# Kernel optimization log

Measured on AMD Instinct MI355X. Metric: run time of the kernel, lower is better.

Reference implementation:

```python
import jax, jax.numpy as jnp
import numpy as np

B, N, E, D, H, OUT = 4, 20000, 320000, 64, 128, 64
EPS = 1e-5


def layernorm(x, g, b):
    m = x.mean(-1, keepdims=True)
    v = x.var(-1, keepdims=True)
    return (x - m) / jnp.sqrt(v + EPS) * g + b


def setup_inputs() -> dict:
    key = jax.random.key(0)
    ks = jax.random.split(key, 20)
    nodes = jax.random.normal(ks[0], (B, N, D), jnp.float32)
    edges = jax.random.randint(ks[1], (B, E, 2), 0, N)
    edge_weights = jax.random.uniform(ks[2], (B, E), dtype=jnp.float32)
    s = 0.05
    inp = {"nodes": nodes, "edges": edges, "edge_weights": edge_weights}
    dims = [(3 * D, H), (H, H), (H, H), (H, OUT)]
    for i, (di, do) in enumerate(dims, start=1):
        inp[f"W{i}"] = jax.random.normal(ks[2 + 4 * i], (di, do), jnp.float32) * s
        inp[f"b{i}"] = jax.random.normal(ks[3 + 4 * i], (do,), jnp.float32) * s
        inp[f"g{i}"] = 1.0 + jax.random.normal(ks[4 + 4 * i], (do,), jnp.float32) * s
        inp[f"t{i}"] = jax.random.normal(ks[5 + 4 * i], (do,), jnp.float32) * s
    return inp


def reference(nodes, edges, edge_weights,
              W1, b1, g1, t1, W2, b2, g2, t2,
              W3, b3, g3, t3, W4, b4, g4, t4):
    # gather source/dest node features per edge: [B, E, D]
    src_idx = edges[..., 0]  # [B, E]
    dst_idx = edges[..., 1]  # [B, E]
    w = edge_weights[..., None]  # [B, E, 1]
    in_feat = jnp.take_along_axis(nodes, src_idx[..., None], axis=1) * w
    out_feat = jnp.take_along_axis(nodes, dst_idx[..., None], axis=1) * w

    # scatter-sum per node (segment sum over flattened batch*node ids)
    off = jnp.arange(B, dtype=dst_idx.dtype)[:, None] * N
    agg_in = jax.ops.segment_sum(in_feat.reshape(B * E, D),
                                 (dst_idx + off).reshape(-1),
                                 num_segments=B * N).reshape(B, N, D)
    agg_out = jax.ops.segment_sum(out_feat.reshape(B * E, D),
                                  (src_idx + off).reshape(-1),
                                  num_segments=B * N).reshape(B, N, D)

    x = jnp.concatenate([agg_in, agg_out, nodes], axis=2)  # [B, N, 3D]
    x = jnp.tanh(layernorm(x @ W1 + b1, g1, t1))
    x = jnp.tanh(layernorm(x @ W2 + b2, g2, t2))
    x = jnp.tanh(layernorm(x @ W3 + b3, g3, t3))
    x = jnp.tanh(layernorm(x @ W4 + b4, g4, t4))
    return x
```

## Files before the change

### kernel.cpp

```cpp
#include <hip/hip_runtime.h>
#include <math.h>

constexpr int Bc   = 4;
constexpr int Nc   = 20000;
constexpr int Ec   = 320000;
constexpr int Dc   = 64;
constexpr int ROWS = Bc * Nc;
constexpr int NSL  = 79;
constexpr int NBK  = 2 * Bc * NSL;
constexpr int CAP  = 48;
constexpr int EPW  = 2560;
constexpr int WPB  = 125;
constexpr int NWG  = Bc * WPB;
constexpr int TPW  = 128;
#define EPS 1e-5f

typedef __attribute__((ext_vector_type(8))) _Float16 f16x8;
typedef __attribute__((ext_vector_type(4))) float f32x4;

constexpr int CH32  = 5120;
constexpr int CH4c  = 2560;
constexpr int WQ_L2 = 30720;
constexpr int WQ_L3 = 51200;
constexpr int WQ_L4 = 71680;
constexpr int WQ_TOT = 81920;
constexpr int WPBLK = WQ_TOT / 256;

__global__ __launch_bounds__(256) void prep_all(
    const float* __restrict__ W1, const float* __restrict__ W2,
    const float* __restrict__ W3, const float* __restrict__ W4,
    _Float16* __restrict__ wp,
    const float* __restrict__ nodes, _Float16* __restrict__ n16) {
    const int blk = blockIdx.x;
    const int tid = threadIdx.x;
    if (blk < WPBLK) {
        int idx = blk * 256 + tid;
        const float* W; int DOl, base;
        if (idx < WQ_L2)      { W = W1; DOl = 128; base = 0; }
        else if (idx < WQ_L3) { W = W2; DOl = 128; base = WQ_L2; }
        else if (idx < WQ_L4) { W = W3; DOl = 128; base = WQ_L3; }
        else                  { W = W4; DOl = 64;  base = WQ_L4; }
        int local = idx - base;
        int chsz = DOl * 40;
        int chunk = local / chsz, rem = local - chunk * chsz;
        int col = rem / 40, kk = rem - col * 40;
        int k = chunk * 32 + kk;
        float v = (kk < 32) ? W[(size_t)k * DOl + col] : 0.f;
        wp[idx] = (_Float16)v;
    } else {
        int i = ((blk - WPBLK) * 256 + tid) * 8;
        float4 a = *(const float4*)(nodes + i);
        float4 b = *(const float4*)(nodes + i + 4);
        f16x8 h;
        h[0] = (_Float16)a.x; h[1] = (_Float16)a.y; h[2] = (_Float16)a.z; h[3] = (_Float16)a.w;
        h[4] = (_Float16)b.x; h[5] = (_Float16)b.y; h[6] = (_Float16)b.z; h[7] = (_Float16)b.w;
        *(f16x8*)(n16 + i) = h;
    }
}

__global__ __launch_bounds__(256) void local_bin(
    const int2* __restrict__ edges, const float* __restrict__ ew,
    uint2* __restrict__ staging, int* __restrict__ tblS, int* __restrict__ tblC) {
    __shared__ int cnt[256];
    __shared__ int offs[256];
    __shared__ int wsum[4];
    __shared__ uint2 stg[EPW * 2];

    const int tid = threadIdx.x;
    const int wg  = blockIdx.x;
    const int b   = wg / WPB;
    const int wgl = wg - b * WPB;
    const int base = wg * EPW;
    const int lane = tid & 63, wid = tid >> 6;

    cnt[tid] = 0;
    __syncthreads();

    int2 e[10]; unsigned wb[10];
#pragma unroll
    for (int j = 0; j < 10; ++j) {
        int idx = base + j * 256 + tid;
        e[j]  = edges[idx];
        wb[j] = __float_as_uint(ew[idx]);
    }

#pragma unroll
    for (int j = 0; j < 10; ++j) {
        atomicAdd(&cnt[e[j].y >> 8], 1);
        atomicAdd(&cnt[79 + (e[j].x >> 8)], 1);
    }
    __syncthreads();

    int v = cnt[tid];
    int incl = v;
#pragma unroll
    for (int d = 1; d < 64; d <<= 1) {
        int t = __shfl_up(incl, d, 64);
        if (lane >= d) incl += t;
    }
    if (lane == 63) wsum[wid] = incl;
    __syncthreads();
    int add = 0;
#pragma unroll
    for (int w = 0; w < 4; ++w)
        if (w < wid) add += wsum[w];
    offs[tid] = incl - v + add;
    __syncthreads();

    if (tid < 158) {
        int lb = tid;
        int row = (lb < 79) ? (b * NSL + lb) : (Bc * NSL + b * NSL + (lb - 79));
        tblS[row * TPW + wgl] = offs[lb];
        tblC[row * TPW + wgl] = cnt[lb];
    }
    __syncthreads();

#pragma unroll
    for (int j = 0; j < 10; ++j) {
        int pA = atomicAdd(&offs[e[j].y >> 8], 1);
        stg[pA] = make_uint2(((unsigned)(e[j].y & 255) << 16) | (unsigned)e[j].x, wb[j]);
        int pB = atomicAdd(&offs[79 + (e[j].x >> 8)], 1);
        stg[pB] = make_uint2(((unsigned)(e[j].x & 255) << 16) | (unsigned)e[j].y, wb[j]);
    }
    __syncthreads();

    uint2* outp = staging + (size_t)wg * (EPW * 2);
#pragma unroll
    for (int it = 0; it < 20; ++it)
        outp[it * 256 + tid] = stg[it * 256 + tid];
}

__global__ __launch_bounds__(1024) void sort_bins(
    const uint2* __restrict__ staging,
    const int* __restrict__ tblS, const int* __restrict__ tblC,
    unsigned* __restrict__ list, int* __restrict__ cnt) {
    __shared__ unsigned lds[256 * CAP];
    __shared__ int lcnt[256];
    __shared__ int segS[WPB], segC[WPB];

    const int tid    = threadIdx.x;
    const int bucket = blockIdx.x;
    const int lane   = tid & 63, wid = tid >> 6;

    const int dir   = bucket >= Bc * NSL;
    const int rem   = bucket - dir * Bc * NSL;
    const int b     = rem / NSL;
    const int slice = rem % NSL;
    const int node0 = slice << 8;

    for (int i = tid; i < 256 * CAP; i += 1024) lds[i] = 0u;
    if (tid < 256) lcnt[tid] = 0;
    if (tid < WPB) {
        int st = tblS[bucket * TPW + tid];
        int c  = tblC[bucket * TPW + tid];
        if (st < 0) st = 0; if (st > EPW * 2) st = EPW * 2;
        if (c  < 0) c  = 0; if (c  > EPW * 2 - st) c = EPW * 2 - st;
        segS[tid] = st;
        segC[tid] = c;
    }
    __syncthreads();

#define INSERT(EN)                                                                \
    {                                                                             \
        int local = (EN).x >> 16;                                                 \
        unsigned nbr  = (EN).x & 0xFFFFu;                                         \
        unsigned wtop = ((EN).y + 0x4000u) & 0xFFFF8000u;                         \
        int p = atomicAdd(&lcnt[local], 1);                                       \
        if (p < CAP) lds[local * CAP + p] = wtop | nbr;                           \
    }

    for (int s = wid; s < WPB; s += 32) {
        const int s1 = s + 16;
        const int c0 = segC[s];
        const int c1 = (s1 < WPB) ? segC[s1] : 0;
        const uint2* sp0 = staging + (size_t)(b * WPB + s) * (EPW * 2) + segS[s];
        const uint2* sp1 = (s1 < WPB)
            ? staging + (size_t)(b * WPB + s1) * (EPW * 2) + segS[s1] : sp0;
        uint2 e0, e1;
        const bool v0 = lane < c0, v1 = lane < c1;
        if (v0) e0 = sp0[lane];
        if (v1) e1 = sp1[lane];
        if (v0) INSERT(e0)
        if (v1) INSERT(e1)
        for (int l0 = 64; l0 < c0; l0 += 64)
            if (lane < c0 - l0) { uint2 e = sp0[l0 + lane]; INSERT(e) }
        for (int l0 = 64; l0 < c1; l0 += 64)
            if (lane < c1 - l0) { uint2 e = sp1[l0 + lane]; INSERT(e) }
    }
#undef INSERT
    __syncthreads();

    int nvalid = Nc - node0; if (nvalid > 256) nvalid = 256;
    const int keybase = dir * ROWS + b * Nc + node0;

    if (tid < nvalid) {
        int vv = lcnt[tid];
        cnt[keybase + tid] = vv < CAP ? vv : CAP;
    }
    unsigned* outp = list + (size_t)keybase * CAP;
    const int total = nvalid * CAP;
    for (int i = tid; i < total; i += 1024)
        outp[i] = lds[i];
}

__global__ __launch_bounds__(256) void gather_kernel(
    const _Float16* __restrict__ n16,
    const unsigned* __restrict__ list,
    const int* __restrict__ cnt,
    _Float16* __restrict__ agg16_in, _Float16* __restrict__ agg16_out) {
    const int wid  = __builtin_amdgcn_readfirstlane(threadIdx.x >> 6);
    const int lane = threadIdx.x & 63;
    const int bid  = blockIdx.x;
    const int xcd  = bid & 7;
    const int loc  = bid >> 3;
    const int bn   = xcd * 10000 + loc * 4 + wid;
    const int b    = bn / Nc;
    const _Float16* nb = n16 + (size_t)b * Nc * Dc;

    const int c0 = cnt[bn];
    const int c1 = cnt[ROWS + bn];
    const int cmax = c0 > c1 ? c0 : c1;
    const unsigned* lp0 = list + (size_t)bn * CAP;
    const unsigned* lp1 = list + (size_t)(ROWS + bn) * CAP;
    float accI0 = 0.f, accI1 = 0.f, accO0 = 0.f, accO1 = 0.f;
    for (int i = 0; i < cmax; i += 16) {
        uint4 a0 = *(const uint4*)(lp0 + i);
        uint4 a1 = *(const uint4*)(lp0 + i + 4);
        uint4 a2 = *(const uint4*)(lp0 + i + 8);
        uint4 a3 = *(const uint4*)(lp0 + i + 12);
        uint4 b0 = *(const uint4*)(lp1 + i);
        uint4 b1 = *(const uint4*)(lp1 + i + 4);
        uint4 b2 = *(const uint4*)(lp1 + i + 8);
        uint4 b3 = *(const uint4*)(lp1 + i + 12);
        unsigned evI[16] = {a0.x, a0.y, a0.z, a0.w, a1.x, a1.y, a1.z, a1.w,
                            a2.x, a2.y, a2.z, a2.w, a3.x, a3.y, a3.z, a3.w};
        unsigned evO[16] = {b0.x, b0.y, b0.z, b0.w, b1.x, b1.y, b1.z, b1.w,
                            b2.x, b2.y, b2.z, b2.w, b3.x, b3.y, b3.z, b3.w};
        unsigned sI[16], sO[16];
        float rI[16], rO[16];
#pragma unroll
        for (int j = 0; j < 16; ++j) {
            sI[j] = __builtin_amdgcn_readfirstlane(evI[j]);
            sO[j] = __builtin_amdgcn_readfirstlane(evO[j]);
            rI[j] = (float)(nb + ((size_t)(sI[j] & 0x7FFFu) << 6))[lane];
            rO[j] = (float)(nb + ((size_t)(sO[j] & 0x7FFFu) << 6))[lane];
        }
#pragma unroll
        for (int j = 0; j < 16; j += 2) {
            accI0 = fmaf(rI[j],     __uint_as_float(sI[j]     & 0xFFFF8000u), accI0);
            accI1 = fmaf(rI[j + 1], __uint_as_float(sI[j + 1] & 0xFFFF8000u), accI1);
            accO0 = fmaf(rO[j],     __uint_as_float(sO[j]     & 0xFFFF8000u), accO0);
            accO1 = fmaf(rO[j + 1], __uint_as_float(sO[j + 1] & 0xFFFF8000u), accO1);
        }
    }
    agg16_in[(size_t)bn * Dc + lane]  = (_Float16)(accI0 + accI1);
    agg16_out[(size_t)bn * Dc + lane] = (_Float16)(accO0 + accO1);
}

__device__ inline float fast_tanh(float x) {
    float e = exp2f(x * 2.885390081777927f);
    return 1.0f - 2.0f * __builtin_amdgcn_rcpf(e + 1.0f);
}

__global__ __launch_bounds__(256, 4) void mlp_fused(
    const _Float16* __restrict__ agg16_in,
    const _Float16* __restrict__ agg16_out,
    const _Float16* __restrict__ n16,
    const _Float16* __restrict__ wp,
    const float* __restrict__ b1, const float* __restrict__ g1, const float* __restrict__ t1,
    const float* __restrict__ b2, const float* __restrict__ g2, const float* __restrict__ t2,
    const float* __restrict__ b3, const float* __restrict__ g3, const float* __restrict__ t3,
    const float* __restrict__ b4, const float* __restrict__ g4, const float* __restrict__ t4,
    float* __restrict__ out) {
    constexpr int XS = 136;
    __shared__ __align__(16) _Float16 wbuf[2][CH32];
    __shared__ __align__(16) _Float16 xh[64 * XS];

    const int tid = threadIdx.x;
    const int wv  = tid >> 6;
    const int l   = tid & 63;
    const int lm  = l & 15;
    const int lg  = l >> 4;
    const int rowloc = wv * 16;
    const int arow = blockIdx.x * 64 + rowloc + lm;
    const int koff = lg * 8;

    uint4 s0_ = {}, s1_ = {}, s2_ = {};

#define STAGE_LOAD(OFFH, N4)                                                      \
    {                                                                             \
        const uint4* s_ = (const uint4*)(wp + (OFFH));                            \
        if (tid < (N4))       s0_ = s_[tid];                                      \
        if (tid + 256 < (N4)) s1_ = s_[tid + 256];                                \
        if (tid + 512 < (N4)) s2_ = s_[tid + 512];                                \
    }
#define STAGE_WRITE(BUFI, N4)                                                     \
    {                                                                             \
        uint4* d_ = (uint4*)wbuf[BUFI];                                           \
        if (tid < (N4))       d_[tid] = s0_;                                      \
        if (tid + 256 < (N4)) d_[tid + 256] = s1_;                                \
        if (tid + 512 < (N4)) d_[tid + 512] = s2_;                                \
    }

    f32x4 acc[8] = {};
#define ZERO_ACC                                                                  \
    {                                                                             \
        _Pragma("unroll")                                                         \
        for (int ct = 0; ct < 8; ++ct) acc[ct] = (f32x4){0.f, 0.f, 0.f, 0.f};     \
    }

#define L1_COMPUTE(BUFI, SRC16, SUBK)                                             \
    {                                                                             \
        f16x8 ah = *(const f16x8*)((SRC16) + (size_t)arow * 64 + (SUBK) * 32 + koff); \
        __builtin_amdgcn_s_setprio(1);                                            \
        _Pragma("unroll")                                                         \
        for (int ct = 0; ct < 8; ++ct) {                                          \
            int col = ct * 16 + lm;                                               \
            f16x8 bh = *(const f16x8*)(wbuf[BUFI] + col * 40 + koff);             \
            acc[ct] = __builtin_amdgcn_mfma_f32_16x16x32_f16(ah, bh, acc[ct], 0, 0, 0); \
        }                                                                         \
        __builtin_amdgcn_s_setprio(0);                                            \
    }

#define LX_COMPUTE(BUFI, KIDX, NCTv)                                              \
    {                                                                             \
        f16x8 ah = *(const f16x8*)(xh + (rowloc + lm) * XS + (KIDX) * 32 + koff); \
        __builtin_amdgcn_s_setprio(1);                                            \
        _Pragma("unroll")                                                         \
        for (int ct = 0; ct < NCTv; ++ct) {                                       \
            int col = ct * 16 + lm;                                               \
            f16x8 bh = *(const f16x8*)(wbuf[BUFI] + col * 40 + koff);             \
            acc[ct] = __builtin_amdgcn_mfma_f32_16x16x32_f16(ah, bh, acc[ct], 0, 0, 0); \
        }                                                                         \
        __builtin_amdgcn_s_setprio(0);                                            \
    }

#define EPILOGUE(NCTv, DOv, BIAS, GG, TT, STORE_LDS)                              \
    {                                                                             \
        float s[4] = {0, 0, 0, 0}, ss[4] = {0, 0, 0, 0};                          \
        _Pragma("unroll")                                                         \
        for (int ct = 0; ct < NCTv; ++ct) {                                       \
            float bc = BIAS[ct * 16 + lm];                                        \
            _Pragma("unroll")                                                     \
            for (int r = 0; r < 4; ++r) {                                         \
                float v = acc[ct][r] + bc;                                        \
                acc[ct][r] = v;                                                   \
                s[r] += v; ss[r] += v * v;                                        \
            }                                                                     \
        }                                                                         \
        _Pragma("unroll")                                                         \
        for (int m = 1; m < 16; m <<= 1) {                                        \
            _Pragma("unroll")                                                     \
            for (int r = 0; r < 4; ++r) {                                         \
                s[r]  += __shfl_xor(s[r],  m, 64);                                \
                ss[r] += __shfl_xor(ss[r], m, 64);                                \
            }                                                                     \
        }                                                                         \
        float mean[4], rstd[4];                                                   \
        _Pragma("unroll")                                                         \
        for (int r = 0; r < 4; ++r) {                                             \
            mean[r] = s[r] * (1.0f / DOv);                                        \
            float var = ss[r] * (1.0f / DOv) - mean[r] * mean[r];                 \
            rstd[r] = rsqrtf(var + EPS);                                          \
        }                                                                         \
        _Pragma("unroll")                                                         \
        for (int ct = 0; ct < NCTv; ++ct) {                                       \
            int col = ct * 16 + lm;                                               \
            float gc = GG[col], tc = TT[col];                                     \
            _Pragma("unroll")                                                     \
            for (int r = 0; r < 4; ++r) {                                         \
                float v = (acc[ct][r] - mean[r]) * rstd[r] * gc + tc;             \
                float th = fast_tanh(v);                                          \
                int row = rowloc + lg * 4 + r;                                    \
                if (STORE_LDS) {                                                  \
                    xh[row * XS + col] = (_Float16)th;                            \
                } else {                                                          \
                    out[(size_t)(blockIdx.x * 64 + row) * 64 + col] = th;         \
                }                                                                 \
            }                                                                     \
        }                                                                         \
    }

    STAGE_LOAD(0, 640)
    STAGE_WRITE(0, 640)
    __syncthreads();

    STAGE_LOAD(CH32, 640)
    L1_COMPUTE(0, agg16_in, 0)
    STAGE_WRITE(1, 640)
    __syncthreads();

    STAGE_LOAD(2 * CH32, 640)
    L1_COMPUTE(1, agg16_in, 1)
    STAGE_WRITE(0, 640)
    __syncthreads();

    STAGE_LOAD(3 * CH32, 640)
    L1_COMPUTE(0, agg16_out, 0)
    STAGE_WRITE(1, 640)
    __syncthreads();

    STAGE_LOAD(4 * CH32, 640)
    L1_COMPUTE(1, agg16_out, 1)
    STAGE_WRITE(0, 640)
    __syncthreads();

    STAGE_LOAD(5 * CH32, 640)
    L1_COMPUTE(0, n16, 0)
    STAGE_WRITE(1, 640)
    __syncthreads();

    STAGE_LOAD(WQ_L2, 640)
    L1_COMPUTE(1, n16, 1)
    EPILOGUE(8, 128, b1, g1, t1, 1)
    STAGE_WRITE(0, 640)
    __syncthreads();
    ZERO_ACC

    STAGE_LOAD(WQ_L2 + CH32, 640)
    LX_COMPUTE(0, 0, 8)
    STAGE_WRITE(1, 640)
    __syncthreads();

    STAGE_LOAD(WQ_L2 + 2 * CH32, 640)
    LX_COMPUTE(1, 1, 8)
    STAGE_WRITE(0, 640)
    __syncthreads();

    STAGE_LOAD(WQ_L2 + 3 * CH32, 640)
    LX_COMPUTE(0, 2, 8)
    STAGE_WRITE(1, 640)
    __syncthreads();

    STAGE_LOAD(WQ_L3, 640)
    LX_COMPUTE(1, 3, 8)
    EPILOGUE(8, 128, b2, g2, t2, 1)
    STAGE_WRITE(0, 640)
    __syncthreads();
    ZERO_ACC

    STAGE_LOAD(WQ_L3 + CH32, 640)
    LX_COMPUTE(0, 0, 8)
    STAGE_WRITE(1, 640)
    __syncthreads();

    STAGE_LOAD(WQ_L3 + 2 * CH32, 640)
    LX_COMPUTE(1, 1, 8)
    STAGE_WRITE(0, 640)
    __syncthreads();

    STAGE_LOAD(WQ_L3 + 3 * CH32, 640)
    LX_COMPUTE(0, 2, 8)
    STAGE_WRITE(1, 640)
    __syncthreads();

    STAGE_LOAD(WQ_L4, 320)
    LX_COMPUTE(1, 3, 8)
    EPILOGUE(8, 128, b3, g3, t3, 1)
    STAGE_WRITE(0, 320)
    __syncthreads();
    ZERO_ACC

    STAGE_LOAD(WQ_L4 + CH4c, 320)
    LX_COMPUTE(0, 0, 4)
    STAGE_WRITE(1, 320)
    __syncthreads();

    STAGE_LOAD(WQ_L4 + 2 * CH4c, 320)
    LX_COMPUTE(1, 1, 4)
    STAGE_WRITE(0, 320)
    __syncthreads();

    STAGE_LOAD(WQ_L4 + 3 * CH4c, 320)
    LX_COMPUTE(0, 2, 4)
    STAGE_WRITE(1, 320)
    __syncthreads();

    LX_COMPUTE(1, 3, 4)
    EPILOGUE(4, 64, b4, g4, t4, 0)

#undef STAGE_LOAD
#undef STAGE_WRITE
#undef ZERO_ACC
#undef L1_COMPUTE
#undef LX_COMPUTE
#undef EPILOGUE
}

extern "C" void kernel_launch(void* const* d_in, const int* in_sizes, int n_in,
                              void* d_out, int out_size, void* d_ws, size_t ws_size,
                              hipStream_t stream) {
    const float* nodes = (const float*)d_in[0];
    const int*   edges = (const int*)d_in[1];
    const float* ew    = (const float*)d_in[2];
    const float* W1 = (const float*)d_in[3];
    const float* b1 = (const float*)d_in[4];
    const float* g1 = (const float*)d_in[5];
    const float* t1 = (const float*)d_in[6];
    const float* W2 = (const float*)d_in[7];
    const float* b2 = (const float*)d_in[8];
    const float* g2 = (const float*)d_in[9];
    const float* t2 = (const float*)d_in[10];
    const float* W3 = (const float*)d_in[11];
    const float* b3 = (const float*)d_in[12];
    const float* g3 = (const float*)d_in[13];
    const float* t3 = (const float*)d_in[14];
    const float* W4 = (const float*)d_in[15];
    const float* b4 = (const float*)d_in[16];
    const float* g4 = (const float*)d_in[17];
    const float* t4 = (const float*)d_in[18];

    float* out = (float*)d_out;

    const size_t AGG = (size_t)ROWS * Dc;
    float* ws      = (float*)d_ws;

    uint2*    staging = (uint2*)ws;
    _Float16* agg16_in  = (_Float16*)ws;
    _Float16* agg16_out = (_Float16*)(ws + AGG / 2);
    int*      tblS    = (int*)(ws + AGG);
    int*      tblC    = (int*)(ws + AGG) + (size_t)NBK * TPW;
    _Float16* n16     = (_Float16*)(ws + AGG + 262144);
    unsigned* list    = (unsigned*)(ws + 2 * AGG);
    int*      cnt     = (int*)(ws + 2 * AGG + (size_t)ROWS * 2 * CAP);

    _Float16* wp = (_Float16*)(ws + 4 * AGG);

    const int2* e2 = (const int2*)edges;

    prep_all<<<WPBLK + (int)(AGG / 2048), 256, 0, stream>>>(
        W1, W2, W3, W4, wp, nodes, n16);

    local_bin<<<NWG, 256, 0, stream>>>(e2, ew, staging, tblS, tblC);
    sort_bins<<<NBK, 1024, 0, stream>>>(staging, tblS, tblC, list, cnt);

    gather_kernel<<<ROWS / 4, 256, 0, stream>>>(n16, list, cnt,
                                                agg16_in, agg16_out);

    mlp_fused<<<ROWS / 64, 256, 0, stream>>>(
        agg16_in, agg16_out, n16, wp,
        b1, g1, t1, b2, g2, t2, b3, g3, t3, b4, g4, t4, out);
}
```

Before: 113.1 us.

## Fuse bin sorting with neighbor gather so adjacency lists stay in LDS

Merges the sort_bins and gather_kernel launches into one sort_gather kernel. Each block builds its 256-node adjacency lists in LDS and then immediately gathers neighbor features from them, removing the global write and re-read of the list/cnt buffers and one launch. Block indices are remapped so the 8 batch/direction pairs are interleaved across XCDs, and the aggregation buffers move to a separate workspace region. In exchange, the gather now runs inside only 632 large 1024-thread blocks that hold a big LDS allocation, so it has less parallelism and occupancy than the old 20000-block gather, and each wave handles 16 nodes with two accumulators instead of four.

```diff
diff --git a/kernel.cpp b/kernel.cpp
--- a/kernel.cpp
+++ b/kernel.cpp
@@ -130,23 +130,24 @@
         outp[it * 256 + tid] = stg[it * 256 + tid];
 }
 
-__global__ __launch_bounds__(1024) void sort_bins(
+__global__ __launch_bounds__(1024) void sort_gather(
     const uint2* __restrict__ staging,
     const int* __restrict__ tblS, const int* __restrict__ tblC,
-    unsigned* __restrict__ list, int* __restrict__ cnt) {
+    const _Float16* __restrict__ n16,
+    _Float16* __restrict__ agg16_in, _Float16* __restrict__ agg16_out) {
     __shared__ unsigned lds[256 * CAP];
     __shared__ int lcnt[256];
     __shared__ int segS[WPB], segC[WPB];
 
-    const int tid    = threadIdx.x;
-    const int bucket = blockIdx.x;
-    const int lane   = tid & 63, wid = tid >> 6;
-
-    const int dir   = bucket >= Bc * NSL;
-    const int rem   = bucket - dir * Bc * NSL;
-    const int b     = rem / NSL;
-    const int slice = rem % NSL;
+    const int tid  = threadIdx.x;
+    const int lane = tid & 63, wid = tid >> 6;
+
+    const int pair  = blockIdx.x & 7;
+    const int slice = blockIdx.x >> 3;
+    const int dir   = pair >> 2;
+    const int b     = pair & 3;
     const int node0 = slice << 8;
+    const int bucket = dir * (Bc * NSL) + b * NSL + slice;
 
     for (int i = tid; i < 256 * CAP; i += 1024) lds[i] = 0u;
     if (tid < 256) lcnt[tid] = 0;
@@ -191,70 +192,38 @@
     __syncthreads();
 
     int nvalid = Nc - node0; if (nvalid > 256) nvalid = 256;
-    const int keybase = dir * ROWS + b * Nc + node0;
-
-    if (tid < nvalid) {
-        int vv = lcnt[tid];
-        cnt[keybase + tid] = vv < CAP ? vv : CAP;
-    }
-    unsigned* outp = list + (size_t)keybase * CAP;
-    const int total = nvalid * CAP;
-    for (int i = tid; i < total; i += 1024)
-        outp[i] = lds[i];
-}
-
-__global__ __launch_bounds__(256) void gather_kernel(
-    const _Float16* __restrict__ n16,
-    const unsigned* __restrict__ list,
-    const int* __restrict__ cnt,
-    _Float16* __restrict__ agg16_in, _Float16* __restrict__ agg16_out) {
-    const int wid  = __builtin_amdgcn_readfirstlane(threadIdx.x >> 6);
-    const int lane = threadIdx.x & 63;
-    const int bid  = blockIdx.x;
-    const int xcd  = bid & 7;
-    const int loc  = bid >> 3;
-    const int bn   = xcd * 10000 + loc * 4 + wid;
-    const int b    = bn / Nc;
     const _Float16* nb = n16 + (size_t)b * Nc * Dc;
-
-    const int c0 = cnt[bn];
-    const int c1 = cnt[ROWS + bn];
-    const int cmax = c0 > c1 ? c0 : c1;
-    const unsigned* lp0 = list + (size_t)bn * CAP;
-    const unsigned* lp1 = list + (size_t)(ROWS + bn) * CAP;
-    float accI0 = 0.f, accI1 = 0.f, accO0 = 0.f, accO1 = 0.f;
-    for (int i = 0; i < cmax; i += 16) {
-        uint4 a0 = *(const uint4*)(lp0 + i);
-        uint4 a1 = *(const uint4*)(lp0 + i + 4);
-        uint4 a2 = *(const uint4*)(lp0 + i + 8);
-        uint4 a3 = *(const uint4*)(lp0 + i + 12);
-        uint4 b0 = *(const uint4*)(lp1 + i);
-        uint4 b1 = *(const uint4*)(lp1 + i + 4);
-        uint4 b2 = *(const uint4*)(lp1 + i + 8);
-        uint4 b3 = *(const uint4*)(lp1 + i + 12);
-        unsigned evI[16] = {a0.x, a0.y, a0.z, a0.w, a1.x, a1.y, a1.z, a1.w,
-                            a2.x, a2.y, a2.z, a2.w, a3.x, a3.y, a3.z, a3.w};
-        unsigned evO[16] = {b0.x, b0.y, b0.z, b0.w, b1.x, b1.y, b1.z, b1.w,
-                            b2.x, b2.y, b2.z, b2.w, b3.x, b3.y, b3.z, b3.w};
-        unsigned sI[16], sO[16];
-        float rI[16], rO[16];
-#pragma unroll
-        for (int j = 0; j < 16; ++j) {
-            sI[j] = __builtin_amdgcn_readfirstlane(evI[j]);
-            sO[j] = __builtin_amdgcn_readfirstlane(evO[j]);
-            rI[j] = (float)(nb + ((size_t)(sI[j] & 0x7FFFu) << 6))[lane];
-            rO[j] = (float)(nb + ((size_t)(sO[j] & 0x7FFFu) << 6))[lane];
+    _Float16* dstbase = (dir ? agg16_out : agg16_in) + ((size_t)b * Nc + node0) * Dc;
+
+    for (int nn = 0; nn < 16; nn += 2) {
+        const int nA = wid * 16 + nn;
+        const int nB = nA + 1;
+        int cA = lcnt[nA]; if (cA > CAP) cA = CAP;
+        int cB = lcnt[nB]; if (cB > CAP) cB = CAP;
+        const int cmax = cA > cB ? cA : cB;
+        float accA = 0.f, accB = 0.f;
+        for (int i = 0; i < cmax; i += 16) {
+            unsigned sA[16], sB[16];
+            float rA[16], rB[16];
+#pragma unroll
+            for (int j = 0; j < 16; ++j) {
+                sA[j] = __builtin_amdgcn_readfirstlane(lds[nA * CAP + i + j]);
+                sB[j] = __builtin_amdgcn_readfirstlane(lds[nB * CAP + i + j]);
+            }
+#pragma unroll
+            for (int j = 0; j < 16; ++j) {
+                rA[j] = (float)(nb + ((size_t)(sA[j] & 0x7FFFu) << 6))[lane];
+                rB[j] = (float)(nb + ((size_t)(sB[j] & 0x7FFFu) << 6))[lane];
+            }
+#pragma unroll
+            for (int j = 0; j < 16; ++j) {
+                accA = fmaf(rA[j], __uint_as_float(sA[j] & 0xFFFF8000u), accA);
+                accB = fmaf(rB[j], __uint_as_float(sB[j] & 0xFFFF8000u), accB);
+            }
         }
-#pragma unroll
-        for (int j = 0; j < 16; j += 2) {
-            accI0 = fmaf(rI[j],     __uint_as_float(sI[j]     & 0xFFFF8000u), accI0);
-            accI1 = fmaf(rI[j + 1], __uint_as_float(sI[j + 1] & 0xFFFF8000u), accI1);
-            accO0 = fmaf(rO[j],     __uint_as_float(sO[j]     & 0xFFFF8000u), accO0);
-            accO1 = fmaf(rO[j + 1], __uint_as_float(sO[j + 1] & 0xFFFF8000u), accO1);
-        }
-    }
-    agg16_in[(size_t)bn * Dc + lane]  = (_Float16)(accI0 + accI1);
-    agg16_out[(size_t)bn * Dc + lane] = (_Float16)(accO0 + accO1);
+        if (nA < nvalid) dstbase[(size_t)nA * Dc + lane] = (_Float16)accA;
+        if (nB < nvalid) dstbase[(size_t)nB * Dc + lane] = (_Float16)accB;
+    }
 }
 
 __device__ inline float fast_tanh(float x) {
@@ -516,13 +485,11 @@
     float* ws      = (float*)d_ws;
 
     uint2*    staging = (uint2*)ws;
-    _Float16* agg16_in  = (_Float16*)ws;
-    _Float16* agg16_out = (_Float16*)(ws + AGG / 2);
     int*      tblS    = (int*)(ws + AGG);
     int*      tblC    = (int*)(ws + AGG) + (size_t)NBK * TPW;
     _Float16* n16     = (_Float16*)(ws + AGG + 262144);
-    unsigned* list    = (unsigned*)(ws + 2 * AGG);
-    int*      cnt     = (int*)(ws + 2 * AGG + (size_t)ROWS * 2 * CAP);
+    _Float16* agg16_in  = (_Float16*)(ws + 2 * AGG);
+    _Float16* agg16_out = (_Float16*)(ws + 2 * AGG) + AGG;
 
     _Float16* wp = (_Float16*)(ws + 4 * AGG);
 
@@ -532,10 +499,9 @@
         W1, W2, W3, W4, wp, nodes, n16);
 
     local_bin<<<NWG, 256, 0, stream>>>(e2, ew, staging, tblS, tblC);
-    sort_bins<<<NBK, 1024, 0, stream>>>(staging, tblS, tblC, list, cnt);
-
-    gather_kernel<<<ROWS / 4, 256, 0, stream>>>(n16, list, cnt,
-                                                agg16_in, agg16_out);
+
+    sort_gather<<<NBK, 1024, 0, stream>>>(staging, tblS, tblC, n16,
+                                          agg16_in, agg16_out);
 
     mlp_fused<<<ROWS / 64, 256, 0, stream>>>(
         agg16_in, agg16_out, n16, wp,
```

After: 114.1 us. Within noise of the previous version (+0.9%).
